# Kernel tuning notes

Hardware: AMD Instinct MI355X
Metric: run time of the kernel (lower is better)

The kernel has to match this reference:

```python
import jax, jax.numpy as jnp
import numpy as np

BIG = 1e30
B, Hh, Ww, DM = 8, 64, 64, 128
DI = 2 * DM          # d_inner
RR = -(-DM // 16)    # dt_rank = ceil(DM/16)
HID = 512


def _ln(x, g, b, eps):
    mu = jnp.mean(x, -1, keepdims=True)
    var = jnp.mean((x - mu) ** 2, -1, keepdims=True)
    return (x - mu) * jax.lax.rsqrt(var + eps) * g + b


def _silu(x):
    return x * jax.nn.sigmoid(x)


def _grid_weights(f):
    # f: [D,H,W]; MST edge weights exp(-cosine_sim) on 4-connected grid, BIG = invalid
    def cos(a, b):
        num = jnp.sum(a * b, 0)
        den = jnp.maximum(jnp.linalg.norm(a, axis=0) * jnp.linalg.norm(b, axis=0), 1e-8)
        return num / den
    wr = jnp.pad(jnp.exp(-cos(f[:, :, :-1], f[:, :, 1:])), ((0, 0), (0, 1)), constant_values=BIG).reshape(-1)
    wd = jnp.pad(jnp.exp(-cos(f[:, :-1, :], f[:, 1:, :])), ((0, 1), (0, 0)), constant_values=BIG).reshape(-1)
    return wr, wd


def _mst(wr, wd, H, W):
    # Prim's minimum spanning tree on HxW grid. Addition order is a valid
    # topological order (parent precedes child), equivalent to the BFS sort
    # for the order-invariant tree-scan aggregation.
    L = H * W

    def body(t, st):
        dist, par, intree, order = st
        v = jnp.argmin(jnp.where(intree, BIG, dist)).astype(jnp.int32)
        intree = intree.at[v].set(True)
        order = order.at[t].set(v)
        r, c = v // W, v % W
        for u, valid, w in (
            (v + 1, c < W - 1, wr[v]),
            (v - 1, c > 0, wr[jnp.clip(v - 1, 0, L - 1)]),
            (v + W, r < H - 1, wd[v]),
            (v - W, r > 0, wd[jnp.clip(v - W, 0, L - 1)]),
        ):
            uc = jnp.clip(u, 0, L - 1)
            better = valid & (~intree[uc]) & (w < dist[uc])
            dist = dist.at[uc].set(jnp.where(better, w, dist[uc]))
            par = par.at[uc].set(jnp.where(better, v, par[uc]))
        return dist, par, intree, order

    st0 = (jnp.full((L,), BIG, jnp.float32).at[0].set(-1.0),
           jnp.zeros((L,), jnp.int32),
           jnp.zeros((L,), bool),
           jnp.zeros((L,), jnp.int32))
    _, par, _, order = jax.lax.fori_loop(0, L, body, st0)
    return order, par


def _tree_scan(feat, ew, order, par):
    # feat, ew: [D,L]. Two-pass tree filter: out[i] = sum_j prod_{e in path(i,j)} w_e * f[j]
    vs = order[1:]
    ps = par[vs]

    def up_step(up, vp):
        v, p = vp
        return up.at[:, p].add(ew[:, v] * up[:, v]), None

    up, _ = jax.lax.scan(up_step, feat, (vs[::-1], ps[::-1]))
    root = order[0]
    out0 = jnp.zeros_like(up).at[:, root].set(up[:, root])

    def down_step(out, vp):
        v, p = vp
        w = ew[:, v]
        return out.at[:, v].set(up[:, v] + w * (out[:, p] - w * up[:, v])), None

    out, _ = jax.lax.scan(down_step, out0, (vs, ps))
    return out


def reference(x, ln1_g, ln1_b, ln2_g, ln2_b, w_in, conv_w, x_weight, dt_weight,
              dt_bias, a_logs, ds, hn_g, hn_b, on_g, on_b, w_out,
              mlp_w1, mlp_b1, mlp_w2, mlp_b2):
    Bb, H, W, _ = x.shape
    L = H * W
    # --- TreeScan branch ---
    h = _ln(x, ln1_g, ln1_b, 1e-6)
    xc, z = jnp.split(h @ w_in.T, 2, -1)
    z = _silu(z)
    xc = jnp.transpose(xc, (0, 3, 1, 2))                      # [B,Di,H,W]
    xc = _silu(jax.lax.conv_general_dilated(
        xc, conv_w, (1, 1), ((1, 1), (1, 1)),
        dimension_numbers=('NCHW', 'OIHW', 'NCHW'),
        feature_group_count=xc.shape[1]))
    Di = xc.shape[1]
    xs = xc.reshape(Bb, Di, L)
    R = dt_weight.shape[2]
    x_dbl = jnp.einsum('bdl,cd->bcl', xs, x_weight[0])        # [B,R+2,L]
    dts, Bs, Cs = x_dbl[:, :R], x_dbl[:, R:R + 1], x_dbl[:, R + 1:]
    dts = jnp.einsum('brl,dr->bdl', dts, dt_weight[0])
    dts = jax.nn.softplus(dts + dt_bias.reshape(-1)[None, :, None])
    As = -jnp.exp(a_logs.reshape(-1).astype(jnp.float32))     # N=1
    deltaA = jnp.exp(dts * As[None, :, None])                 # per-channel edge weights
    feat_in = dts * Bs * xs                                   # deltaB * x (K=N=1)
    # MST + topological sort under no-grad (matches torch.no_grad())
    f4t = jax.lax.stop_gradient(xs).reshape(Bb, Di, H, W)
    wr, wd = jax.vmap(_grid_weights)(f4t)
    order, par = jax.vmap(lambda a, b: _mst(a, b, H, W))(wr, wd)
    feat_out = jax.vmap(_tree_scan)(feat_in, deltaA, order, par)  # [B,Di,L]
    ho = _ln(jnp.swapaxes(feat_out, 1, 2), hn_g, hn_b, 1e-5)      # h_norm
    y = jnp.swapaxes(ho * jnp.swapaxes(Cs, 1, 2), 1, 2)           # multiply by Cs (N=1)
    y = y + ds[None, :, None] * xs                                # D skip
    y = _ln(jnp.swapaxes(y, 1, 2), on_g, on_b, 1e-5).reshape(Bb, H, W, Di)
    scan_out = (y * z) @ w_out.T
    # --- residual + MLP ---
    x1 = x + scan_out
    h2 = _ln(x1, ln2_g, ln2_b, 1e-6)
    mlp = jax.nn.gelu(h2 @ mlp_w1.T + mlp_b1) @ mlp_w2.T + mlp_b2
    return x1 + mlp


def setup_inputs():
    key = jax.random.key(0)
    ks = jax.random.split(key, 12)

    def rn(k, shape, s):
        return jax.random.normal(k, shape, jnp.float32) * s

    dt = jnp.exp(jax.random.uniform(ks[10], (DI,)) * (np.log(0.1) - np.log(0.001)) + np.log(0.001))
    dt_bias = (dt + jnp.log(-jnp.expm1(-dt)))[None]  # inverse-softplus init
    return {
        'x': rn(ks[0], (B, Hh, Ww, DM), 1.0),
        'ln1_g': jnp.ones((DM,)), 'ln1_b': jnp.zeros((DM,)),
        'ln2_g': jnp.ones((DM,)), 'ln2_b': jnp.zeros((DM,)),
        'w_in': rn(ks[1], (2 * DI, DM), DM ** -0.5),
        'conv_w': rn(ks[2], (DI, 1, 3, 3), 1.0 / 3.0),
        'x_weight': rn(ks[3], (1, RR + 2, DI), DI ** -0.5),
        'dt_weight': rn(ks[4], (1, DI, RR), RR ** -0.5),
        'dt_bias': dt_bias,
        'a_logs': jnp.zeros((DI, 1)),
        'ds': jnp.ones((DI,)),
        'hn_g': jnp.ones((DI,)), 'hn_b': jnp.zeros((DI,)),
        'on_g': jnp.ones((DI,)), 'on_b': jnp.zeros((DI,)),
        'w_out': rn(ks[5], (DM, DI), DI ** -0.5),
        'mlp_w1': rn(ks[6], (HID, DM), DM ** -0.5),
        'mlp_b1': jnp.zeros((HID,)),
        'mlp_w2': rn(ks[7], (DM, HID), HID ** -0.5),
        'mlp_b2': jnp.zeros((DM,)),
    }
```

## Files before the change

### kernel.cpp

```cpp
#include <hip/hip_runtime.h>
#include <hip/hip_bf16.h>
#include <cstdint>

#define BIGF 1e30f
constexpr int LB   = 4096;
constexpr int NB   = 8;
constexpr int MROWS = NB * LB;
constexpr int LSP  = 4104;

__device__ __forceinline__ float warp_sum(float v) {
#pragma unroll
  for (int off = 32; off; off >>= 1) v += __shfl_xor(v, off);
  return v;
}

__device__ __forceinline__ float block_sum256(float v) {
  __shared__ float sm[4];
  v = warp_sum(v);
  __syncthreads();
  if ((threadIdx.x & 63) == 0) sm[threadIdx.x >> 6] = v;
  __syncthreads();
  return sm[0] + sm[1] + sm[2] + sm[3];
}

__global__ __launch_bounds__(256) void ln128_kernel(
    const float* __restrict__ X, const float* __restrict__ g,
    const float* __restrict__ bb, float* __restrict__ O, float eps) {
  int wave = threadIdx.x >> 6, lane = threadIdx.x & 63;
  int row = blockIdx.x * 4 + wave;
  const float* xr = X + (size_t)row * 128;
  float x0 = xr[lane], x1 = xr[lane + 64];
  float mu = warp_sum(x0 + x1) * (1.0f / 128.0f);
  float d0 = x0 - mu, d1 = x1 - mu;
  float var = warp_sum(d0 * d0 + d1 * d1) * (1.0f / 128.0f);
  float s = 1.0f / sqrtf(var + eps);
  float* orow = O + (size_t)row * 128;
  orow[lane]      = d0 * s * g[lane]      + bb[lane];
  orow[lane + 64] = d1 * s * g[lane + 64] + bb[lane + 64];
}

template<int EPI>
__global__ __launch_bounds__(256) void gemm_kernel(
    const float* __restrict__ A, const float* __restrict__ W,
    float* __restrict__ C, float* __restrict__ C2,
    const float* __restrict__ bias, const float* __restrict__ addsrc,
    int M, int N, int K) {
  __shared__ float As[32][68];
  __shared__ float Bs[32][68];
  int t = threadIdx.x;
  int tx = t & 15, ty = t >> 4;
  int bm = blockIdx.y * 64, bn = blockIdx.x * 64;
  float acc[4][4] = {};
  for (int k0 = 0; k0 < K; k0 += 32) {
#pragma unroll
    for (int hh = 0; hh < 2; ++hh) {
      int q = t + hh * 256;
      int r = q >> 3, kc = q & 7;
      float4 a4 = reinterpret_cast<const float4*>(A + (size_t)(bm + r) * K + k0)[kc];
      float4 b4 = reinterpret_cast<const float4*>(W + (size_t)(bn + r) * K + k0)[kc];
      As[kc * 4 + 0][r] = a4.x; As[kc * 4 + 1][r] = a4.y;
      As[kc * 4 + 2][r] = a4.z; As[kc * 4 + 3][r] = a4.w;
      Bs[kc * 4 + 0][r] = b4.x; Bs[kc * 4 + 1][r] = b4.y;
      Bs[kc * 4 + 2][r] = b4.z; Bs[kc * 4 + 3][r] = b4.w;
    }
    __syncthreads();
#pragma unroll
    for (int kk = 0; kk < 32; ++kk) {
      float4 av = *reinterpret_cast<const float4*>(&As[kk][ty * 4]);
      float4 bv = *reinterpret_cast<const float4*>(&Bs[kk][tx * 4]);
      float aa[4] = {av.x, av.y, av.z, av.w};
      float bbv[4] = {bv.x, bv.y, bv.z, bv.w};
#pragma unroll
      for (int i = 0; i < 4; ++i)
#pragma unroll
        for (int j = 0; j < 4; ++j) acc[i][j] += aa[i] * bbv[j];
    }
    __syncthreads();
  }
#pragma unroll
  for (int i = 0; i < 4; ++i) {
    int m = bm + ty * 4 + i;
#pragma unroll
    for (int j = 0; j < 4; ++j) {
      int n = bn + tx * 4 + j;
      float v = acc[i][j];
      if (EPI == 2) {
        C[(size_t)m * N + n] = v + addsrc[(size_t)m * N + n];
      } else if (EPI == 4) {
        C[(size_t)m * N + n] = v + bias[n] + addsrc[(size_t)m * N + n];
      }
    }
  }
}

template<int EPI>
__global__ __launch_bounds__(256) void gemm128_kernel(
    const float* __restrict__ A, const float* __restrict__ W,
    float* __restrict__ C, float* __restrict__ C2,
    const float* __restrict__ bias, int M, int N, int K) {
  __shared__ float As[32][132];
  __shared__ float Bs[32][132];
  int t = threadIdx.x;
  int tx = t & 15, ty = t >> 4;
  int bm = blockIdx.y * 128, bn = blockIdx.x * 128;
  float acc[8][8] = {};
  for (int k0 = 0; k0 < K; k0 += 32) {
#pragma unroll
    for (int hh = 0; hh < 4; ++hh) {
      int q = t + hh * 256;
      int r = q >> 3, kc = q & 7;
      float4 a4 = *reinterpret_cast<const float4*>(A + (size_t)(bm + r) * K + k0 + kc * 4);
      float4 b4 = *reinterpret_cast<const float4*>(W + (size_t)(bn + r) * K + k0 + kc * 4);
      As[kc * 4 + 0][r] = a4.x; As[kc * 4 + 1][r] = a4.y;
      As[kc * 4 + 2][r] = a4.z; As[kc * 4 + 3][r] = a4.w;
      Bs[kc * 4 + 0][r] = b4.x; Bs[kc * 4 + 1][r] = b4.y;
      Bs[kc * 4 + 2][r] = b4.z; Bs[kc * 4 + 3][r] = b4.w;
    }
    __syncthreads();
#pragma unroll
    for (int kk = 0; kk < 32; ++kk) {
      float4 a0 = *reinterpret_cast<const float4*>(&As[kk][ty * 4]);
      float4 a1 = *reinterpret_cast<const float4*>(&As[kk][64 + ty * 4]);
      float4 b0 = *reinterpret_cast<const float4*>(&Bs[kk][tx * 4]);
      float4 b1 = *reinterpret_cast<const float4*>(&Bs[kk][64 + tx * 4]);
      float aa[8] = {a0.x, a0.y, a0.z, a0.w, a1.x, a1.y, a1.z, a1.w};
      float bb2[8] = {b0.x, b0.y, b0.z, b0.w, b1.x, b1.y, b1.z, b1.w};
#pragma unroll
      for (int i = 0; i < 8; ++i)
#pragma unroll
        for (int j = 0; j < 8; ++j) acc[i][j] += aa[i] * bb2[j];
    }
    __syncthreads();
  }
#pragma unroll
  for (int i = 0; i < 8; ++i) {
    int m = bm + (i >> 2) * 64 + ty * 4 + (i & 3);
#pragma unroll
    for (int j = 0; j < 8; ++j) {
      int n = bn + (j >> 2) * 64 + tx * 4 + (j & 3);
      float v = acc[i][j];
      if (EPI == 1) {
        if (n < 256) C[(size_t)m * 256 + n] = v;
        else C2[(size_t)m * 256 + (n - 256)] = v / (1.0f + __expf(-v));
      } else if (EPI == 3) {
        float u = v + bias[n];
        float xg = 1.5957691216057308f * (u + 0.044715f * u * u * u);
        C[(size_t)m * N + n] = u / (1.0f + __expf(-xg));
      }
    }
  }
}

__global__ __launch_bounds__(256) void convfeat_kernel(
    const float* __restrict__ xcpre, const float* __restrict__ cw,
    const float* __restrict__ xw, const float* __restrict__ dtw,
    const float* __restrict__ dtb, const float* __restrict__ alogs,
    float* __restrict__ xs, float* __restrict__ dAt, float* __restrict__ featt,
    float* __restrict__ Cs, float* __restrict__ ssq) {
  int m = blockIdx.x;
  int d = threadIdx.x;
  int l = m & (LB - 1), b = m >> 12;
  int r = l >> 6, c = l & 63;
  float acc = 0.f;
#pragma unroll
  for (int ky = 0; ky < 3; ++ky) {
    int rr = r + ky - 1;
    if (rr < 0 || rr > 63) continue;
#pragma unroll
    for (int kx = 0; kx < 3; ++kx) {
      int cc = c + kx - 1;
      if (cc < 0 || cc > 63) continue;
      int ml = (b << 12) + (rr << 6) + cc;
      acc += xcpre[(size_t)ml * 256 + d] * cw[d * 9 + ky * 3 + kx];
    }
  }
  float xv = acc / (1.0f + __expf(-acc));
  xs[(size_t)m * 256 + d] = xv;
  float p[11];
#pragma unroll
  for (int i = 0; i < 10; ++i) p[i] = xv * xw[i * 256 + d];
  p[10] = xv * xv;
  __shared__ float sm[4][11];
#pragma unroll
  for (int i = 0; i < 11; ++i) p[i] = warp_sum(p[i]);
  int wv = d >> 6;
  if ((d & 63) == 0) {
    for (int i = 0; i < 11; ++i) sm[wv][i] = p[i];
  }
  __syncthreads();
  float red[11];
#pragma unroll
  for (int i = 0; i < 11; ++i) red[i] = sm[0][i] + sm[1][i] + sm[2][i] + sm[3][i];
  float xdt = dtb[d];
#pragma unroll
  for (int rr2 = 0; rr2 < 8; ++rr2) xdt += red[rr2] * dtw[d * 8 + rr2];
  float sp = fmaxf(xdt, 0.f) + __logf(1.0f + __expf(-fabsf(xdt)));
  float As_ = -__expf(alogs[d]);
  size_t tidx = ((size_t)(b * 64 + (d >> 2)) * 4096 + l) * 4 + (d & 3);
  dAt[tidx]   = __expf(sp * As_);
  featt[tidx] = sp * red[8] * xv;
  if (d == 0) { Cs[m] = red[9]; ssq[m] = red[10]; }
}

__global__ __launch_bounds__(256) void gridw_kernel(
    const float* __restrict__ xs, const float* __restrict__ ssq,
    float* __restrict__ wrg, float* __restrict__ wdg) {
  int m = blockIdx.x, d = threadIdx.x;
  int l = m & (LB - 1);
  int r = l >> 6, c = l & 63;
  float a = xs[(size_t)m * 256 + d];
  float br = (c < 63) ? xs[(size_t)(m + 1) * 256 + d] : 0.f;
  float bd = (r < 63) ? xs[(size_t)(m + 64) * 256 + d] : 0.f;
  float s1 = warp_sum(a * br);
  float s2 = warp_sum(a * bd);
  __shared__ float sm[4][2];
  int wv = d >> 6;
  if ((d & 63) == 0) { sm[wv][0] = s1; sm[wv][1] = s2; }
  __syncthreads();
  if (d == 0) {
    float dotr = sm[0][0] + sm[1][0] + sm[2][0] + sm[3][0];
    float dotd = sm[0][1] + sm[1][1] + sm[2][1] + sm[3][1];
    float na = sqrtf(ssq[m]);
    float wrv = BIGF, wdv = BIGF;
    if (c < 63) { float den = fmaxf(na * sqrtf(ssq[m + 1]), 1e-8f);  wrv = expf(-(dotr / den)); }
    if (r < 63) { float den = fmaxf(na * sqrtf(ssq[m + 64]), 1e-8f); wdv = expf(-(dotd / den)); }
    wrg[m] = wrv; wdg[m] = wdv;
  }
}

__global__ __launch_bounds__(1024) void mst_kernel(
    const float* __restrict__ wr_g, const float* __restrict__ wd_g,
    unsigned int* __restrict__ topo_g, int* __restrict__ levs_g) {
  __shared__ int pool[24592];
  __shared__ unsigned char flagR[4096];
  __shared__ unsigned char flagD[4096];
  __shared__ int ncomp_s;
  __shared__ int wred[16];
  int b = blockIdx.x, tid = threadIdx.x;
  float* wrs = (float*)pool;
  float* wds = (float*)(pool + 4096);
  int* comp = pool + 8192;
  int* lnk  = pool + 12288;
  unsigned int* bestw = (unsigned int*)(pool + 16384);
  int* beste = pool + 20480;
  const float* wrb = wr_g + b * 4096;
  const float* wdb = wd_g + b * 4096;
  for (int k = 0; k < 4; ++k) {
    int i = tid + k * 1024;
    wrs[i] = wrb[i]; wds[i] = wdb[i];
    comp[i] = i; flagR[i] = 0; flagD[i] = 0;
  }
  __syncthreads();
  for (int phase = 0; phase < 13; ++phase) {
    for (int k = 0; k < 4; ++k) {
      int c = tid + k * 1024;
      bestw[c] = 0xFFFFFFFFu; beste[c] = 0x7FFFFFFF; lnk[c] = c;
    }
    if (tid == 0) ncomp_s = 0;
    __syncthreads();
    for (int k = 0; k < 8; ++k) {
      int e = tid + k * 1024;
      int v = e & 4095;
      bool isR = e < 4096;
      int c = v & 63, r = v >> 6;
      bool valid = isR ? (c < 63) : (r < 63);
      if (valid) {
        int u = isR ? v + 1 : v + 64;
        int ca = comp[v], cb = comp[u];
        if (ca != cb) {
          unsigned wbits = __float_as_uint(isR ? wrs[v] : wds[v]);
          atomicMin(&bestw[ca], wbits);
          atomicMin(&bestw[cb], wbits);
        }
      }
    }
    __syncthreads();
    for (int k = 0; k < 8; ++k) {
      int e = tid + k * 1024;
      int v = e & 4095;
      bool isR = e < 4096;
      int c = v & 63, r = v >> 6;
      bool valid = isR ? (c < 63) : (r < 63);
      if (valid) {
        int u = isR ? v + 1 : v + 64;
        int ca = comp[v], cb = comp[u];
        if (ca != cb) {
          unsigned wbits = __float_as_uint(isR ? wrs[v] : wds[v]);
          if (wbits == bestw[ca]) atomicMin(&beste[ca], e);
          if (wbits == bestw[cb]) atomicMin(&beste[cb], e);
        }
      }
    }
    __syncthreads();
    for (int k = 0; k < 4; ++k) {
      int cc = tid + k * 1024;
      int e = beste[cc];
      if (e != 0x7FFFFFFF) {
        int v = e & 4095;
        bool isR = e < 4096;
        int u = isR ? v + 1 : v + 64;
        if (isR) flagR[v] = 1; else flagD[v] = 1;
        int ca = comp[v], cb = comp[u];
        lnk[cc] = (ca == cc) ? cb : ca;
      }
    }
    __syncthreads();
    for (int k = 0; k < 4; ++k) {
      int cc = tid + k * 1024;
      int l = lnk[cc];
      if (l != cc && lnk[l] == cc && cc < l) lnk[cc] = cc;
    }
    __syncthreads();
    for (int it = 0; it < 12; ++it) {
      for (int k = 0; k < 4; ++k) {
        int cc = tid + k * 1024;
        lnk[cc] = lnk[lnk[cc]];
      }
      __syncthreads();
    }
    for (int k = 0; k < 4; ++k) {
      int i = tid + k * 1024;
      comp[i] = lnk[comp[i]];
      if (comp[i] == i) atomicAdd(&ncomp_s, 1);
    }
    __syncthreads();
    if (ncomp_s <= 1) break;
    __syncthreads();
  }
  unsigned short* nxt = (unsigned short*)pool;
  short*          dsv = (short*)(pool + 8200);
  int* par = pool + 16400;
  int* dep = pool + 20496;
  const int NIL = 16384;
  unsigned short rn[16];
  int rd[16];
  int validm = 0;
  for (int k = 0; k < 4; ++k) { int i = tid + k * 1024; par[i] = 0; dep[i] = 0; }
#pragma unroll
  for (int k = 0; k < 16; ++k) {
    int a = tid + k * 1024;
    int u = a >> 2, d = a & 3;
    int c = u & 63, r = u >> 6;
    int mu = 0;
    if (r > 0  && flagD[u - 64]) mu |= 1;
    if (c > 0  && flagR[u - 1])  mu |= 2;
    if (c < 63 && flagR[u])      mu |= 4;
    if (r < 63 && flagD[u])      mu |= 8;
    unsigned short nx = NIL; short dv = 0;
    if (mu & (1 << d)) {
      validm |= 1 << k;
      int v = u + ((d == 0) ? -64 : (d == 1) ? -1 : (d == 2) ? 1 : 64);
      int cv = v & 63, rv = v >> 6;
      int mv = 0;
      if (rv > 0  && flagD[v - 64]) mv |= 1;
      if (cv > 0  && flagR[v - 1])  mv |= 2;
      if (cv < 63 && flagR[v])      mv |= 4;
      if (rv < 63 && flagD[v])      mv |= 8;
      int din = 3 - d;
      int hi = mv >> (din + 1);
      int dn = hi ? (din + __ffs(hi)) : (__ffs(mv) - 1);
      int nxv = v * 4 + dn;
      int m0 = (flagR[0] ? 4 : 0) | (flagD[0] ? 8 : 0);
      int a0 = __ffs(m0) - 1;
      if (v == 0 && nxv == a0) nxv = NIL;
      nx = (unsigned short)nxv;
      dv = 1;
    }
    nxt[a] = nx; dsv[a] = dv;
    rn[k] = nx; rd[k] = dv;
  }
  if (tid == 0) { nxt[NIL] = NIL; dsv[NIL] = 0; }
  __syncthreads();
#pragma unroll 1
  for (int it = 0; it < 13; ++it) {
    unsigned short nn[16]; short nd[16];
#pragma unroll
    for (int k = 0; k < 16; ++k) { nn[k] = nxt[rn[k]]; nd[k] = dsv[rn[k]]; }
    __syncthreads();
#pragma unroll
    for (int k = 0; k < 16; ++k) {
      int a = tid + k * 1024;
      rd[k] += nd[k];
      rn[k] = nn[k];
      nxt[a] = rn[k]; dsv[a] = (short)rd[k];
    }
    __syncthreads();
  }
#pragma unroll
  for (int k = 0; k < 16; ++k) if (validm & (1 << k)) {
    int a = tid + k * 1024;
    int u = a >> 2, d = a & 3;
    int v = u + ((d == 0) ? -64 : (d == 1) ? -1 : (d == 2) ? 1 : 64);
    int rb = v * 4 + (3 - d);
    if (rd[k] > (int)dsv[rb]) par[v] = u;
  }
  __syncthreads();
#pragma unroll
  for (int k = 0; k < 16; ++k) {
    int a = tid + k * 1024;
    int u = a >> 2, d = a & 3;
    unsigned short nx = NIL; short dv = 0;
    if (validm & (1 << k)) {
      int v = u + ((d == 0) ? -64 : (d == 1) ? -1 : (d == 2) ? 1 : 64);
      int cv = v & 63, rv = v >> 6;
      int mv = 0;
      if (rv > 0  && flagD[v - 64]) mv |= 1;
      if (cv > 0  && flagR[v - 1])  mv |= 2;
      if (cv < 63 && flagR[v])      mv |= 4;
      if (rv < 63 && flagD[v])      mv |= 8;
      int din = 3 - d;
      int hi = mv >> (din + 1);
      int dn = hi ? (din + __ffs(hi)) : (__ffs(mv) - 1);
      int nxv = v * 4 + dn;
      int m0 = (flagR[0] ? 4 : 0) | (flagD[0] ? 8 : 0);
      int a0 = __ffs(m0) - 1;
      if (v == 0 && nxv == a0) nxv = NIL;
      nx = (unsigned short)nxv;
      dv = (par[v] == u) ? (short)1 : (short)-1;
    }
    nxt[a] = nx; dsv[a] = dv;
    rn[k] = nx; rd[k] = dv;
  }
  __syncthreads();
#pragma unroll 1
  for (int it = 0; it < 13; ++it) {
    unsigned short nn[16]; short nd[16];
#pragma unroll
    for (int k = 0; k < 16; ++k) { nn[k] = nxt[rn[k]]; nd[k] = dsv[rn[k]]; }
    __syncthreads();
#pragma unroll
    for (int k = 0; k < 16; ++k) {
      int a = tid + k * 1024;
      rd[k] += nd[k];
      rn[k] = nn[k];
      nxt[a] = rn[k]; dsv[a] = (short)rd[k];
    }
    __syncthreads();
  }
#pragma unroll
  for (int k = 0; k < 16; ++k) if (validm & (1 << k)) {
    int a = tid + k * 1024;
    int u = a >> 2, d = a & 3;
    int v = u + ((d == 0) ? -64 : (d == 1) ? -1 : (d == 2) ? 1 : 64);
    if (par[v] == u) dep[v] = 1 - rd[k];
  }
  __syncthreads();
  int md = 0;
  for (int k = 0; k < 4; ++k) md = max(md, dep[tid + k * 1024]);
#pragma unroll
  for (int off = 32; off; off >>= 1) md = max(md, __shfl_xor(md, off));
  if ((tid & 63) == 0) wred[tid >> 6] = md;
  __syncthreads();
  if (tid == 0) {
    int m = 0;
    for (int i = 0; i < 16; ++i) m = max(m, wred[i]);
    wred[0] = m;
  }
  __syncthreads();
  int maxd = wred[0];
  __syncthreads();
  int* cnt  = pool;
  int* offs = pool + 4096;
  for (int k = 0; k < 4; ++k) cnt[tid + k * 1024] = 0;
  __syncthreads();
  for (int k = 0; k < 4; ++k) atomicAdd(&cnt[dep[tid + k * 1024]], 1);
  __syncthreads();
  int base4 = tid * 4;
  int c0 = cnt[base4], c1 = cnt[base4 + 1], c2 = cnt[base4 + 2], c3 = cnt[base4 + 3];
  int tsum = c0 + c1 + c2 + c3;
  int lane = tid & 63, wid = tid >> 6;
  int iv = tsum;
  for (int off = 1; off < 64; off <<= 1) {
    int n = __shfl_up(iv, off);
    if (lane >= off) iv += n;
  }
  if (lane == 63) wred[wid] = iv;
  __syncthreads();
  if (tid == 0) {
    int acc = 0;
    for (int i = 0; i < 16; ++i) { int t = wred[i]; wred[i] = acc; acc += t; }
  }
  __syncthreads();
  int excl = iv - tsum + wred[wid];
  offs[base4]     = excl;
  offs[base4 + 1] = excl + c0;
  offs[base4 + 2] = excl + c0 + c1;
  offs[base4 + 3] = excl + c0 + c1 + c2;
  __syncthreads();
  for (int idx = tid; idx <= maxd; idx += 1024) levs_g[b * LSP + idx] = offs[idx];
  if (tid == 0) {
    levs_g[b * LSP + maxd + 1] = 4096;
    levs_g[b * LSP + 4098] = maxd + 1;
  }
  __syncthreads();
  for (int k = 0; k < 4; ++k) {
    int v2 = tid + k * 1024;
    int pos = atomicAdd(&offs[dep[v2]], 1);
    int c = v2 & 63, r = v2 >> 6;
    unsigned msk = 0;
    if (r > 0  && par[v2 - 64] == v2) msk |= 1;
    if (c > 0  && par[v2 - 1]  == v2) msk |= 2;
    if (c < 63 && par[v2 + 1]  == v2) msk |= 4;
    if (r < 63 && par[v2 + 64] == v2) msk |= 8;
    topo_g[b * 4096 + pos] =
        (unsigned)v2 | (msk << 12) | ((unsigned)par[v2] << 16);
  }
}

__global__ __launch_bounds__(64) void scan_kernel(
    float* __restrict__ buft, const float* __restrict__ ewt,
    const unsigned int* __restrict__ topo_g, const int* __restrict__ levs_g) {
  __shared__ float acc[16384];
  __shared__ unsigned short lvs[4104];
  int bid = blockIdx.x;
  int b = bid >> 6, cg = bid & 63;
  int lane = threadIdx.x;
  int ch = lane & 3, slot = lane >> 2;
  int nlev = levs_g[b * LSP + 4098];
  size_t fbase = (size_t)(b * 64 + cg) * 16384;
  const float4* bt4 = reinterpret_cast<const float4*>(buft + fbase);
  const float*  ewf = ewt + fbase;
  const float4* et4 = reinterpret_cast<const float4*>(ewf);
  const unsigned int* tp = topo_g + b * 4096;
  float4* acc4 = reinterpret_cast<float4*>(acc);
  float wsum = 0.f;
  for (int n = lane; n < 4096; n += 64) {
    acc4[n] = bt4[n];
    float4 ev = et4[n];
    wsum += ev.x + ev.y + ev.z + ev.w;
  }
  asm volatile("" :: "v"(wsum));
  for (int i = lane; i <= nlev; i += 64) lvs[i] = (unsigned short)levs_g[b * LSP + i];
  __syncthreads();
  if (nlev > 1) {
    int lev0 = nlev - 1;
    int jA = lvs[lev0] + slot, eA = lvs[lev0 + 1];
    unsigned tA = tp[jA < 4096 ? jA : 4095];
    float elA = ewf[(tA & 4095) * 4 + ch];
    int jB = 0, eB = 0; unsigned tB = 0; float elB = 0.f;
    if (lev0 - 1 >= 1) {
      jB = lvs[lev0 - 1] + slot; eB = lvs[lev0];
      tB = tp[jB < 4096 ? jB : 4095];
      elB = ewf[(tB & 4095) * 4 + ch];
    }
    int jC = 0, eC = 0; unsigned tC = 0;
    if (lev0 - 2 >= 1) {
      jC = lvs[lev0 - 2] + slot; eC = lvs[lev0 - 1];
      tC = tp[jC < 4096 ? jC : 4095];
    }
    for (int lev = lev0; lev >= 1; --lev) {
      float elC = 0.f;
      if (lev - 2 >= 1) elC = ewf[(tC & 4095) * 4 + ch];
      int jD = 0, eD = 0; unsigned tD = 0;
      if (lev - 3 >= 1) {
        jD = lvs[lev - 3] + slot; eD = lvs[lev - 2];
        tD = tp[jD < 4096 ? jD : 4095];
      }
      if (jA < eA) {
        int vA = tA & 4095, pA = (tA >> 16) & 4095;
        float a = acc[vA * 4 + ch];
        atomicAdd(&acc[pA * 4 + ch], elA * a);
        for (int j = jA + 16; j < eA; j += 16) {
          unsigned t = tp[j];
          int v = t & 4095, p = (t >> 16) & 4095;
          float e = ewf[v * 4 + ch];
          float av = acc[v * 4 + ch];
          atomicAdd(&acc[p * 4 + ch], e * av);
        }
      }
      __builtin_amdgcn_wave_barrier();
      jA = jB; eA = eB; tA = tB; elA = elB;
      jB = jC; eB = eC; tB = tC; elB = elC;
      jC = jD; eC = eD; tC = tD;
    }
  }
  __builtin_amdgcn_wave_barrier();
  if (nlev > 1) {
    int jA = lvs[1] + slot, eA = lvs[2];
    unsigned tA = tp[jA < 4096 ? jA : 4095];
    float elA = ewf[(tA & 4095) * 4 + ch];
    int jB = 0, eB = 0; unsigned tB = 0; float elB = 0.f;
    if (2 < nlev) {
      jB = lvs[2] + slot; eB = lvs[3];
      tB = tp[jB < 4096 ? jB : 4095];
      elB = ewf[(tB & 4095) * 4 + ch];
    }
    int jC = 0, eC = 0; unsigned tC = 0;
    if (3 < nlev) {
      jC = lvs[3] + slot; eC = lvs[4];
      tC = tp[jC < 4096 ? jC : 4095];
    }
    for (int lev = 1; lev < nlev; ++lev) {
      float elC = 0.f;
      if (lev + 2 < nlev) elC = ewf[(tC & 4095) * 4 + ch];
      int jD = 0, eD = 0; unsigned tD = 0;
      if (lev + 3 < nlev) {
        jD = lvs[lev + 3] + slot; eD = lvs[lev + 4];
        tD = tp[jD < 4096 ? jD : 4095];
      }
      if (jA < eA) {
        int vA = tA & 4095, pA = (tA >> 16) & 4095;
        float uv = acc[vA * 4 + ch];
        float pb = acc[pA * 4 + ch];
        acc[vA * 4 + ch] = uv + elA * (pb - elA * uv);
        for (int j = jA + 16; j < eA; j += 16) {
          unsigned t = tp[j];
          int v = t & 4095, p = (t >> 16) & 4095;
          float e = ewf[v * 4 + ch];
          float uvv = acc[v * 4 + ch];
          float pbv = acc[p * 4 + ch];
          acc[v * 4 + ch] = uvv + e * (pbv - e * uvv);
        }
      }
      __builtin_amdgcn_wave_barrier();
      jA = jB; eA = eB; tA = tB; elA = elB;
      jB = jC; eB = eC; tB = tC; elB = elC;
      jC = jD; eC = eD; tC = tD;
    }
  }
  __syncthreads();
  float4* bw4 = reinterpret_cast<float4*>(buft + fbase);
  for (int n = lane; n < 4096; n += 64) bw4[n] = acc4[n];
}

__global__ __launch_bounds__(256) void post_kernel(
    const float* __restrict__ buft, const float* __restrict__ Cs,
    const float* __restrict__ xs, const float* __restrict__ ds,
    const float* __restrict__ hng, const float* __restrict__ hnb,
    const float* __restrict__ ong, const float* __restrict__ onb,
    float* __restrict__ zya) {
  int m = blockIdx.x, d = threadIdx.x;
  int b = m >> 12, l = m & (LB - 1);
  size_t idx = (size_t)m * 256 + d;
  float fo = buft[((size_t)(b * 64 + (d >> 2)) * 4096 + l) * 4 + (d & 3)];
  float mu = block_sum256(fo) * (1.f / 256.f);
  float dv = fo - mu;
  float var = block_sum256(dv * dv) * (1.f / 256.f);
  float ho = dv * (1.0f / sqrtf(var + 1e-5f)) * hng[d] + hnb[d];
  float y = ho * Cs[m] + ds[d] * xs[idx];
  float mu2 = block_sum256(y) * (1.f / 256.f);
  float dy = y - mu2;
  float var2 = block_sum256(dy * dy) * (1.f / 256.f);
  float y2 = dy * (1.0f / sqrtf(var2 + 1e-5f)) * ong[d] + onb[d];
  zya[idx] = y2 * zya[idx];
}

extern "C" void kernel_launch(void* const* d_in, const int* in_sizes, int n_in,
                              void* d_out, int out_size, void* d_ws, size_t ws_size,
                              hipStream_t stream) {
  (void)in_sizes; (void)n_in; (void)out_size; (void)ws_size;
  const float* x      = (const float*)d_in[0];
  const float* ln1g   = (const float*)d_in[1];
  const float* ln1b   = (const float*)d_in[2];
  const float* ln2g   = (const float*)d_in[3];
  const float* ln2b   = (const float*)d_in[4];
  const float* w_in   = (const float*)d_in[5];
  const float* conv_w = (const float*)d_in[6];
  const float* xw     = (const float*)d_in[7];
  const float* dtw    = (const float*)d_in[8];
  const float* dtb    = (const float*)d_in[9];
  const float* alogs  = (const float*)d_in[10];
  const float* dsv    = (const float*)d_in[11];
  const float* hng    = (const float*)d_in[12];
  const float* hnb    = (const float*)d_in[13];
  const float* ong    = (const float*)d_in[14];
  const float* onb    = (const float*)d_in[15];
  const float* w_out  = (const float*)d_in[16];
  const float* mw1    = (const float*)d_in[17];
  const float* mb1    = (const float*)d_in[18];
  const float* mw2    = (const float*)d_in[19];
  const float* mb2    = (const float*)d_in[20];

  char* ws = (char*)d_ws;
  float* h    = (float*)(ws + 0);
  float* z    = (float*)(ws + 16777216);
  float* xcp  = (float*)(ws + 50331648);
  float* xs   = (float*)(ws + 83886080);
  float* dAt  = (float*)(ws + 117440512);
  float* featt= (float*)(ws + 150994944);
  float* Cs   = (float*)(ws + 184549376);
  float* ssq  = (float*)(ws + 184680448);
  float* wr   = (float*)(ws + 184811520);
  float* wd   = (float*)(ws + 184942592);
  unsigned int* topo32 = (unsigned int*)(ws + 185073664);
  int*   levs = (int*)(ws + 185335808);
  float* midg = xs;
  float* x1   = h;
  float* h2   = xcp;

  ln128_kernel<<<MROWS / 4, 256, 0, stream>>>(x, ln1g, ln1b, h, 1e-6f);
  gemm128_kernel<1><<<dim3(4, 256), 256, 0, stream>>>(h, w_in, xcp, z, nullptr,
                                                      MROWS, 512, 128);
  convfeat_kernel<<<MROWS, 256, 0, stream>>>(xcp, conv_w, xw, dtw, dtb, alogs,
                                             xs, dAt, featt, Cs, ssq);
  gridw_kernel<<<MROWS, 256, 0, stream>>>(xs, ssq, wr, wd);
  mst_kernel<<<NB, 1024, 0, stream>>>(wr, wd, topo32, levs);
  scan_kernel<<<512, 64, 0, stream>>>(featt, dAt, topo32, levs);
  post_kernel<<<MROWS, 256, 0, stream>>>(featt, Cs, xs, dsv, hng, hnb, ong, onb, z);
  gemm_kernel<2><<<dim3(2, 512), 256, 0, stream>>>(z, w_out, x1, nullptr, nullptr, x,
                                                   MROWS, 128, 256);
  ln128_kernel<<<MROWS / 4, 256, 0, stream>>>(x1, ln2g, ln2b, h2, 1e-6f);
  gemm128_kernel<3><<<dim3(4, 256), 256, 0, stream>>>(h2, mw1, midg, nullptr, mb1,
                                                      MROWS, 512, 128);
  gemm_kernel<4><<<dim3(2, 512), 256, 0, stream>>>(midg, mw2, (float*)d_out, nullptr,
                                                   mb2, x1, MROWS, 128, 512);
}
```

Measured before the change: 847.9 us.

## Fuse LayerNorm into GEMM prologue and make post kernel wave-per-row

Removes both standalone LayerNorm kernels by computing per-row mean and rstd at the start of the 128-wide GEMM and normalizing A tiles as they are loaded into shared memory. The post kernel now handles one row per 64-lane wave using float4 loads and shuffle-only reductions, instead of one row per 256-thread block with shared-memory block reductions. This saves two launches, the intermediate h buffer round trips, and the barriers in post. In exchange each GEMM block rereads its A rows for the statistics, and the four column blocks recompute the same statistics.

```diff
diff --git a/kernel.cpp b/kernel.cpp
--- a/kernel.cpp
+++ b/kernel.cpp
@@ -12,31 +12,6 @@
 #pragma unroll
   for (int off = 32; off; off >>= 1) v += __shfl_xor(v, off);
   return v;
-}
-
-__device__ __forceinline__ float block_sum256(float v) {
-  __shared__ float sm[4];
-  v = warp_sum(v);
-  __syncthreads();
-  if ((threadIdx.x & 63) == 0) sm[threadIdx.x >> 6] = v;
-  __syncthreads();
-  return sm[0] + sm[1] + sm[2] + sm[3];
-}
-
-__global__ __launch_bounds__(256) void ln128_kernel(
-    const float* __restrict__ X, const float* __restrict__ g,
-    const float* __restrict__ bb, float* __restrict__ O, float eps) {
-  int wave = threadIdx.x >> 6, lane = threadIdx.x & 63;
-  int row = blockIdx.x * 4 + wave;
-  const float* xr = X + (size_t)row * 128;
-  float x0 = xr[lane], x1 = xr[lane + 64];
-  float mu = warp_sum(x0 + x1) * (1.0f / 128.0f);
-  float d0 = x0 - mu, d1 = x1 - mu;
-  float var = warp_sum(d0 * d0 + d1 * d1) * (1.0f / 128.0f);
-  float s = 1.0f / sqrtf(var + eps);
-  float* orow = O + (size_t)row * 128;
-  orow[lane]      = d0 * s * g[lane]      + bb[lane];
-  orow[lane + 64] = d1 * s * g[lane + 64] + bb[lane + 64];
 }
 
 template<int EPI>
@@ -94,15 +69,40 @@
 }
 
 template<int EPI>
-__global__ __launch_bounds__(256) void gemm128_kernel(
+__global__ __launch_bounds__(256) void gemm128ln_kernel(
     const float* __restrict__ A, const float* __restrict__ W,
     float* __restrict__ C, float* __restrict__ C2,
-    const float* __restrict__ bias, int M, int N, int K) {
+    const float* __restrict__ bias, const float* __restrict__ lng,
+    const float* __restrict__ lnb, int M, int N, int K) {
   __shared__ float As[32][132];
   __shared__ float Bs[32][132];
+  __shared__ float mu_s[128], rs_s[128], g_s[128], b_s[128];
   int t = threadIdx.x;
   int tx = t & 15, ty = t >> 4;
   int bm = blockIdx.y * 128, bn = blockIdx.x * 128;
+  {
+    int r = t >> 1, hf = t & 1;
+    const float4* row = reinterpret_cast<const float4*>(A + (size_t)(bm + r) * K + hf * 64);
+    float s = 0.f;
+#pragma unroll
+    for (int i = 0; i < 16; ++i) { float4 v = row[i]; s += v.x + v.y + v.z + v.w; }
+    s += __shfl_xor(s, 1);
+    float mu = s * (1.0f / 128.0f);
+    float sq = 0.f;
+#pragma unroll
+    for (int i = 0; i < 16; ++i) {
+      float4 v = row[i];
+      float d0 = v.x - mu, d1 = v.y - mu, d2 = v.z - mu, d3 = v.w - mu;
+      sq += d0 * d0 + d1 * d1 + d2 * d2 + d3 * d3;
+    }
+    sq += __shfl_xor(sq, 1);
+    if (hf == 0) {
+      mu_s[r] = mu;
+      rs_s[r] = 1.0f / sqrtf(sq * (1.0f / 128.0f) + 1e-6f);
+    }
+    if (t < 128) { g_s[t] = lng[t]; b_s[t] = lnb[t]; }
+  }
+  __syncthreads();
   float acc[8][8] = {};
   for (int k0 = 0; k0 < K; k0 += 32) {
 #pragma unroll
@@ -111,8 +111,12 @@
       int r = q >> 3, kc = q & 7;
       float4 a4 = *reinterpret_cast<const float4*>(A + (size_t)(bm + r) * K + k0 + kc * 4);
       float4 b4 = *reinterpret_cast<const float4*>(W + (size_t)(bn + r) * K + k0 + kc * 4);
-      As[kc * 4 + 0][r] = a4.x; As[kc * 4 + 1][r] = a4.y;
-      As[kc * 4 + 2][r] = a4.z; As[kc * 4 + 3][r] = a4.w;
+      float mu = mu_s[r], rs = rs_s[r];
+      int c0 = k0 + kc * 4;
+      As[kc * 4 + 0][r] = (a4.x - mu) * rs * g_s[c0]     + b_s[c0];
+      As[kc * 4 + 1][r] = (a4.y - mu) * rs * g_s[c0 + 1] + b_s[c0 + 1];
+      As[kc * 4 + 2][r] = (a4.z - mu) * rs * g_s[c0 + 2] + b_s[c0 + 2];
+      As[kc * 4 + 3][r] = (a4.w - mu) * rs * g_s[c0 + 3] + b_s[c0 + 3];
       Bs[kc * 4 + 0][r] = b4.x; Bs[kc * 4 + 1][r] = b4.y;
       Bs[kc * 4 + 2][r] = b4.z; Bs[kc * 4 + 3][r] = b4.w;
     }
@@ -629,20 +633,37 @@
     const float* __restrict__ hng, const float* __restrict__ hnb,
     const float* __restrict__ ong, const float* __restrict__ onb,
     float* __restrict__ zya) {
-  int m = blockIdx.x, d = threadIdx.x;
+  int w = threadIdx.x >> 6, lane = threadIdx.x & 63;
+  int m = blockIdx.x * 4 + w;
   int b = m >> 12, l = m & (LB - 1);
-  size_t idx = (size_t)m * 256 + d;
-  float fo = buft[((size_t)(b * 64 + (d >> 2)) * 4096 + l) * 4 + (d & 3)];
-  float mu = block_sum256(fo) * (1.f / 256.f);
-  float dv = fo - mu;
-  float var = block_sum256(dv * dv) * (1.f / 256.f);
-  float ho = dv * (1.0f / sqrtf(var + 1e-5f)) * hng[d] + hnb[d];
-  float y = ho * Cs[m] + ds[d] * xs[idx];
-  float mu2 = block_sum256(y) * (1.f / 256.f);
-  float dy = y - mu2;
-  float var2 = block_sum256(dy * dy) * (1.f / 256.f);
-  float y2 = dy * (1.0f / sqrtf(var2 + 1e-5f)) * ong[d] + onb[d];
-  zya[idx] = y2 * zya[idx];
+  float4 fo = *reinterpret_cast<const float4*>(
+      buft + ((size_t)(b * 64 + lane) * 4096 + l) * 4);
+  float mu = warp_sum(fo.x + fo.y + fo.z + fo.w) * (1.f / 256.f);
+  float4 dv = make_float4(fo.x - mu, fo.y - mu, fo.z - mu, fo.w - mu);
+  float var = warp_sum(dv.x * dv.x + dv.y * dv.y + dv.z * dv.z + dv.w * dv.w) * (1.f / 256.f);
+  float rs = 1.0f / sqrtf(var + 1e-5f);
+  float4 hg = reinterpret_cast<const float4*>(hng)[lane];
+  float4 hb = reinterpret_cast<const float4*>(hnb)[lane];
+  float csv = Cs[m];
+  float4 dsv4 = reinterpret_cast<const float4*>(ds)[lane];
+  float4 xv = reinterpret_cast<const float4*>(xs + (size_t)m * 256)[lane];
+  float y0 = (dv.x * rs * hg.x + hb.x) * csv + dsv4.x * xv.x;
+  float y1 = (dv.y * rs * hg.y + hb.y) * csv + dsv4.y * xv.y;
+  float y2_ = (dv.z * rs * hg.z + hb.z) * csv + dsv4.z * xv.z;
+  float y3 = (dv.w * rs * hg.w + hb.w) * csv + dsv4.w * xv.w;
+  float mu2 = warp_sum(y0 + y1 + y2_ + y3) * (1.f / 256.f);
+  float d0 = y0 - mu2, d1 = y1 - mu2, d2 = y2_ - mu2, d3 = y3 - mu2;
+  float var2 = warp_sum(d0 * d0 + d1 * d1 + d2 * d2 + d3 * d3) * (1.f / 256.f);
+  float rs2 = 1.0f / sqrtf(var2 + 1e-5f);
+  float4 og = reinterpret_cast<const float4*>(ong)[lane];
+  float4 ob = reinterpret_cast<const float4*>(onb)[lane];
+  float4* zp = reinterpret_cast<float4*>(zya + (size_t)m * 256) + lane;
+  float4 zv = *zp;
+  zv.x = (d0 * rs2 * og.x + ob.x) * zv.x;
+  zv.y = (d1 * rs2 * og.y + ob.y) * zv.y;
+  zv.z = (d2 * rs2 * og.z + ob.z) * zv.z;
+  zv.w = (d3 * rs2 * og.w + ob.w) * zv.w;
+  *zp = zv;
 }
 
 extern "C" void kernel_launch(void* const* d_in, const int* in_sizes, int n_in,
@@ -672,7 +693,7 @@
   const float* mb2    = (const float*)d_in[20];
 
   char* ws = (char*)d_ws;
-  float* h    = (float*)(ws + 0);
+  float* x1   = (float*)(ws + 0);
   float* z    = (float*)(ws + 16777216);
   float* xcp  = (float*)(ws + 50331648);
   float* xs   = (float*)(ws + 83886080);
@@ -685,23 +706,19 @@
   unsigned int* topo32 = (unsigned int*)(ws + 185073664);
   int*   levs = (int*)(ws + 185335808);
   float* midg = xs;
-  float* x1   = h;
-  float* h2   = xcp;
-
-  ln128_kernel<<<MROWS / 4, 256, 0, stream>>>(x, ln1g, ln1b, h, 1e-6f);
-  gemm128_kernel<1><<<dim3(4, 256), 256, 0, stream>>>(h, w_in, xcp, z, nullptr,
-                                                      MROWS, 512, 128);
+
+  gemm128ln_kernel<1><<<dim3(4, 256), 256, 0, stream>>>(x, w_in, xcp, z, nullptr,
+                                                        ln1g, ln1b, MROWS, 512, 128);
   convfeat_kernel<<<MROWS, 256, 0, stream>>>(xcp, conv_w, xw, dtw, dtb, alogs,
                                              xs, dAt, featt, Cs, ssq);
   gridw_kernel<<<MROWS, 256, 0, stream>>>(xs, ssq, wr, wd);
   mst_kernel<<<NB, 1024, 0, stream>>>(wr, wd, topo32, levs);
   scan_kernel<<<512, 64, 0, stream>>>(featt, dAt, topo32, levs);
-  post_kernel<<<MROWS, 256, 0, stream>>>(featt, Cs, xs, dsv, hng, hnb, ong, onb, z);
+  post_kernel<<<MROWS / 4, 256, 0, stream>>>(featt, Cs, xs, dsv, hng, hnb, ong, onb, z);
   gemm_kernel<2><<<dim3(2, 512), 256, 0, stream>>>(z, w_out, x1, nullptr, nullptr, x,
                                                    MROWS, 128, 256);
-  ln128_kernel<<<MROWS / 4, 256, 0, stream>>>(x1, ln2g, ln2b, h2, 1e-6f);
-  gemm128_kernel<3><<<dim3(4, 256), 256, 0, stream>>>(h2, mw1, midg, nullptr, mb1,
-                                                      MROWS, 512, 128);
+  gemm128ln_kernel<3><<<dim3(4, 256), 256, 0, stream>>>(x1, mw1, midg, nullptr, mb1,
+                                                        ln2g, ln2b, MROWS, 512, 128);
   gemm_kernel<4><<<dim3(2, 512), 256, 0, stream>>>(midg, mw2, (float*)d_out, nullptr,
                                                    mb2, x1, MROWS, 128, 512);
 }
```

After: 833.5 us. Within noise of the previous version (-1.7%).
